# Performance work log

Hardware: AMD Instinct MI355X
Metric: run time of the kernel (lower is better)

Reference implementation:

```python
import jax, jax.numpy as jnp
import numpy as np

D = 46      # embed_dim, pinned by hardcoded repeat(1, 46, 1)
H = 256     # hidden_dim
H2 = 128    # hidden_dim // 2
L0 = 4000   # antigen length
L1 = 600    # antibody length
CAT = 250   # heavy/light chain split (catsite)
K_ECA = 3   # ECA conv1d kernel size for C=46
EPS = 1e-5


def _eca(x, w):
    # Standard ECA: global mean over spatial dims, conv1d across channel axis, sigmoid gate.
    spatial = tuple(range(2, x.ndim))
    y = x.mean(axis=spatial)  # [B, C]
    yc = jax.lax.conv_general_dilated(y[:, None, :], w[None, None, :], (1,), 'SAME')[:, 0, :]
    s = jax.nn.sigmoid(yc)
    return x * s.reshape(s.shape + (1,) * len(spatial))


def _bn(x, g, b):
    # BatchNorm2d, training mode (batch statistics, biased variance), affine.
    mu = x.mean(axis=(0, 2, 3), keepdims=True)
    var = ((x - mu) ** 2).mean(axis=(0, 2, 3), keepdims=True)
    return (x - mu) * jax.lax.rsqrt(var + EPS) * g[None, :, None, None] + b[None, :, None, None]


def _conv1x1(x, w, b):
    return jnp.einsum('bcij,oc->boij', x, w) + b[None, :, None, None]


def setup_inputs() -> dict:
    key = jax.random.key(0)
    ks = jax.random.split(key, 10)
    rng = np.random.default_rng(0)
    cdrH = np.sort(rng.choice(np.arange(1, CAT), 50, replace=False))            # CDR positions in heavy chain
    cdrLfull = np.sort(rng.choice(np.arange(CAT + 1, L1 - 1), 50, replace=False))
    inp = {
        'z0': jax.random.normal(ks[0], (1, L0, D), jnp.float32),
        'z1': jax.random.normal(ks[1], (1, L1, D), jnp.float32),
        'w_eca1': jax.random.normal(ks[2], (K_ECA,), jnp.float32) * 0.5,
        'w_eca2': jax.random.normal(ks[3], (K_ECA,), jnp.float32) * 0.5,
        'w_eca3': jax.random.normal(ks[4], (K_ECA,), jnp.float32) * 0.5,
        'w_eca4': jax.random.normal(ks[5], (K_ECA,), jnp.float32) * 0.5,
        'w_eca5': jax.random.normal(ks[6], (K_ECA,), jnp.float32) * 0.5,
        'conv_w': jax.random.normal(ks[7], (H, 2 * D), jnp.float32) / np.sqrt(2 * D).astype(np.float32),
        'conv_b': jnp.zeros((H,), jnp.float32),
        'bn_g': jnp.ones((H,), jnp.float32),
        'bn_b': jnp.zeros((H,), jnp.float32),
        'conv2_w': jax.random.normal(ks[8], (H2, H), jnp.float32) / np.sqrt(H).astype(np.float32),
        'conv2_b': jnp.zeros((H2,), jnp.float32),
        'bn2_g': jnp.ones((H2,), jnp.float32),
        'bn2_b': jnp.zeros((H2,), jnp.float32),
        'cdrHind': jnp.asarray(cdrH, jnp.int32),
        'cdrLind': jnp.asarray(cdrLfull - CAT, jnp.int32),
        'notcdrHind': jnp.asarray(np.setdiff1d(np.arange(CAT), cdrH), jnp.int32),
        'notcdrLind': jnp.asarray(np.setdiff1d(np.arange(CAT, L1 - 1), cdrLfull) - CAT, jnp.int32),
        'catsite': CAT,
    }
    return inp


def reference(z0, z1, w_eca1, w_eca2, w_eca3, w_eca4, w_eca5,
              conv_w, conv_b, bn_g, bn_b, conv2_w, conv2_b, bn2_g, bn2_b,
              cdrHind, cdrLind, notcdrHind, notcdrLind, catsite):
    z0 = z0.transpose(0, 2, 1)   # [1, D, L0]
    z1 = z1.transpose(0, 2, 1)   # [1, D, L1]
    z1H = z1[:, :, :catsite]     # [1, D, LH]
    z1L = z1[:, :, catsite:]     # [1, D, LL]

    z0 = _eca(z0, w_eca1)
    z1H = _eca(z1H, w_eca2)
    z1L = _eca(z1L, w_eca3)

    # Gather CDR / non-CDR residues along the length axis.
    Z1Hcdr = z1H[:, :, cdrHind]        # [1, D, nCH]
    Z1Hnot = z1H[:, :, notcdrHind]     # [1, D, nNH]
    Z1Lcdr = z1L[:, :, cdrLind]
    Z1Lnot = z1L[:, :, notcdrLind]

    # CDR vs non-CDR pairwise |diff|, ECA gate, mean over non-CDR axis.
    z_Hdifcdr = jnp.abs(Z1Hcdr[:, :, :, None] - Z1Hnot[:, :, None, :])  # [1, D, nCH, nNH]
    z1H = _eca(z_Hdifcdr, w_eca4).mean(axis=3)                          # [1, D, nCH]
    z_Ldifcdr = jnp.abs(Z1Lcdr[:, :, :, None] - Z1Lnot[:, :, None, :])
    z1L = _eca(z_Ldifcdr, w_eca5).mean(axis=3)                          # [1, D, nCL]

    # Antigen x heavy-CDR broadcast features.
    z_Hdif = jnp.abs(z0[:, :, :, None] - z1H[:, :, None, :])            # [1, D, L0, nCH]
    z_Hmul = z0[:, :, :, None] * z1H[:, :, None, :]
    z_Hcat = jnp.concatenate([z_Hdif, z_Hmul], axis=1)                  # [1, 2D, L0, nCH]
    z0_mean = z_Hcat.mean(axis=3)                                       # [1, 2D, L0]

    half = z0_mean.shape[1] // 2
    z0_Ldif = z0_mean[:, :half, :]
    z0_Lmul = z0_mean[:, half:, :]
    z_Ldif = jnp.abs(z0_Ldif[:, :, :, None] - z1L[:, :, None, :])       # [1, D, L0, nCL]
    z_Lmul = jnp.abs(z0_Lmul[:, :, :, None] - z1L[:, :, None, :])       # (abs of diff, as in source)
    z_Lcat = jnp.concatenate([z_Ldif, z_Lmul], axis=1)                  # [1, 2D, L0, nCL]

    z_cat = jnp.concatenate([z_Hcat, z_Lcat], axis=3)                   # [1, 2D, L0, nCH+nCL]

    c = jax.nn.relu(_conv1x1(z_cat, conv_w, conv_b))
    c = _bn(c, bn_g, bn_b)
    c = jax.nn.relu(_conv1x1(c, conv2_w, conv2_b))
    c = _bn(c, bn2_g, bn2_b)
    return c
```

## Files before the change

kernel.cpp:

```cpp
#include <hip/hip_runtime.h>
#include <math.h>

#define DD   46
#define LL0  4000
#define LL1  600
#define CATV 250
#define NC   50
#define NJ   100
#define HC   256
#define H2C  128
#define NPOS (LL0*NJ)
#define EPSV 1e-5f
#define NT   64
#define XROW 104
#define C1ROW 268
#define C2PAD 68
#define TILES (NPOS/NT)
#define GRIDP 512

#define W_MEAN0   0
#define W_MEANH   64
#define W_MEANL   128
#define W_RM4     192
#define W_RM5     256
#define W_S1      320
#define W_HBAR    384
#define W_RAWMH   448
#define W_RAWML   2752
#define W_H       5056
#define W_L       7360
#define W_BN1S    9664
#define W_SC1     10176
#define W_BN2S    10688
#define W_SC2     10944
#define W_HBF     11200
#define W_LBF     12400
#define W_AWT     13632
#define W_W1P     589776
#define W_W2BF    602064
#define W_BIAS2   618448

typedef __attribute__((ext_vector_type(8))) short bf8;
typedef __attribute__((ext_vector_type(4))) float f32x4;
typedef __attribute__((ext_vector_type(4))) unsigned u32x4;

__device__ __forceinline__ float sigf(float x){ return 1.0f/(1.0f+__expf(-x)); }

__device__ __forceinline__ unsigned short f2bf(float f){
  unsigned u = __float_as_uint(f);
  return (unsigned short)((u + 0x7FFFu + ((u>>16)&1u)) >> 16);
}
__device__ __forceinline__ unsigned pk2bf(float a, float b){
  return ((unsigned)f2bf(b)<<16) | (unsigned)f2bf(a);
}
__device__ __forceinline__ float bf2f(unsigned short h){
  return __uint_as_float(((unsigned)h)<<16);
}

__device__ float blockReduceSum(float v, float* sm){
  int tid=threadIdx.x;
  sm[tid]=v; __syncthreads();
  for(int s=128;s>0;s>>=1){ if(tid<s) sm[tid]+=sm[tid+s]; __syncthreads(); }
  float r=sm[0]; __syncthreads();
  return r;
}

__global__ void k_prep(const float* __restrict__ conv_w, float* __restrict__ ws){
  int t=blockIdx.x*256+threadIdx.x;
  if(blockIdx.x==0){ for(int e=threadIdx.x;e<1536;e+=256) ws[W_BN1S+e]=0.f; }
  if(t<HC*96){
    int o=t/96, c=t-o*96;
    unsigned short v=0;
    if(c<92){ int d=c>>1, p=c&1; v=f2bf(conv_w[o*92 + (p? 46+d : d)]); }
    ((unsigned short*)(ws+W_W1P))[t]=v;
  }
}

__global__ void k_prep2(const float* __restrict__ conv2_w, const float* __restrict__ conv2_b,
                        float* __restrict__ ws){
  __shared__ float sm[256];
  int o2=blockIdx.x, t=threadIdx.x;
  float wv=conv2_w[o2*HC+t];
  float sc=ws[W_SC1+t], sh=ws[W_SC1+HC+t];
  ((unsigned short*)(ws+W_W2BF))[o2*HC+t]=f2bf(wv*sc);
  float r=blockReduceSum(wv*sh,sm);
  if(t==0) ws[W_BIAS2+o2]=conv2_b[o2]+r;
}

__global__ void k_means(const float* __restrict__ z0, const float* __restrict__ z1,
                        const int* cdrH, const int* notH,
                        const int* cdrL, const int* notL,
                        int nCdrH,int nNotH,int nCdrL,int nNotL, float* ws){
  __shared__ float v[LL1];
  __shared__ float sm[256];
  int d=blockIdx.x, tid=threadIdx.x;
  float s0=0.f; for(int i=tid;i<LL0;i+=256) s0+=z0[i*DD+d];
  for(int k=tid;k<LL1;k+=256) v[k]=z1[k*DD+d];
  float r0=blockReduceSum(s0,sm);
  __syncthreads();
  float sH=0.f; for(int k=tid;k<CATV;k+=256) sH+=v[k];
  float sL=0.f; for(int k=CATV+tid;k<LL1;k+=256) sL+=v[k];
  float rH=blockReduceSum(sH,sm);
  float rL=blockReduceSum(sL,sm);
  float partH=0.f, partL=0.f;
  for(int i=tid;i<nCdrH;i+=256){
    float c=v[cdrH[i]]; float s=0.f;
    for(int j=0;j<nNotH;j++) s+=fabsf(c-v[notH[j]]);
    s/= (float)nNotH;
    ws[W_RAWMH+d*NC+i]=s; partH+=s;
  }
  for(int i=tid;i<nCdrL;i+=256){
    float c=v[CATV+cdrL[i]]; float s=0.f;
    for(int j=0;j<nNotL;j++) s+=fabsf(c-v[CATV+notL[j]]);
    s/= (float)nNotL;
    ws[W_RAWML+d*NC+i]=s; partL+=s;
  }
  float pH=blockReduceSum(partH,sm);
  float pL=blockReduceSum(partL,sm);
  if(tid==0){
    ws[W_MEAN0+d]=r0/(float)LL0;
    ws[W_MEANH+d]=rH/(float)CATV;
    ws[W_MEANL+d]=rL/(float)(LL1-CATV);
    ws[W_RM4+d]=pH/(float)nCdrH;
    ws[W_RM5+d]=pL/(float)nCdrL;
  }
}

__device__ __forceinline__ float conv3(const float* a, int d, const float* w){
  float acc = w[1]*a[d];
  if(d>0)    acc += w[0]*a[d-1];
  if(d<DD-1) acc += w[2]*a[d+1];
  return acc;
}

__global__ void k_scales(const float* w1,const float* w2,const float* w3,
                         const float* w4,const float* w5, float* ws){
  __shared__ float m0[DD], mH[DD], mL[DD];
  __shared__ float s1s[DD],s2s[DD],s3s[DD],s4s[DD],s5s[DD],y4[DD],y5[DD];
  int tid=threadIdx.x;
  if(tid<DD){ m0[tid]=ws[W_MEAN0+tid]; mH[tid]=ws[W_MEANH+tid]; mL[tid]=ws[W_MEANL+tid]; }
  __syncthreads();
  if(tid<DD){
    s1s[tid]=sigf(conv3(m0,tid,w1));
    s2s[tid]=sigf(conv3(mH,tid,w2));
    s3s[tid]=sigf(conv3(mL,tid,w3));
  }
  __syncthreads();
  if(tid<DD){ y4[tid]=s2s[tid]*ws[W_RM4+tid]; y5[tid]=s3s[tid]*ws[W_RM5+tid]; }
  __syncthreads();
  if(tid<DD){
    s4s[tid]=sigf(conv3(y4,tid,w4));
    s5s[tid]=sigf(conv3(y5,tid,w5));
    ws[W_S1+tid]=s1s[tid];
  }
  __syncthreads();
  for(int e=tid;e<DD*NC;e+=256){
    int d=e/NC;
    ws[W_H+e]=s4s[d]*s2s[d]*ws[W_RAWMH+e];
    ws[W_L+e]=s5s[d]*s3s[d]*ws[W_RAWML+e];
  }
  __syncthreads();
  if(tid<DD){
    float s=0.f;
    for(int j=0;j<NC;j++) s+=ws[W_H+tid*NC+j];
    ws[W_HBAR+tid]=s/(float)NC;
  }
  __syncthreads();
  for(int e=tid;e<2400;e+=256){
    int j=e/48, d=e-48*j;
    unsigned short hv=0, lv=0;
    if(d<DD){ hv=f2bf(ws[W_H+d*NC+j]); lv=f2bf(ws[W_L+d*NC+j]); }
    ((unsigned short*)(ws+W_HBF))[e]=hv;
    ((unsigned short*)(ws+W_LBF))[e]=lv;
  }
}

__global__ void k_aw(const float* __restrict__ z0, float* __restrict__ ws){
  int e=blockIdx.x*256+threadIdx.x;
  if(e>=LL0*48) return;
  int i=e/48, d=e-48*i;
  float a=0.f, df=0.f, ml=0.f;
  if(d<DD){
    a = ws[W_S1+d]*z0[i*DD+d];
    float s=0.f;
    #pragma unroll 10
    for(int j=0;j<NC;j++) s+=fabsf(a-ws[W_H+d*NC+j]);
    df = s*(1.0f/(float)NC);
    ml = a*ws[W_HBAR+d];
  }
  ws[W_AWT + i*144 + d]      = a;
  ws[W_AWT + i*144 + 48 + d] = df;
  ws[W_AWT + i*144 + 96 + d] = ml;
}

__device__ __forceinline__ void stage_tables(unsigned short* hT, unsigned short* lT,
                                             const float* __restrict__ ws, int tid){
  for(int e=tid;e<300;e+=256){
    ((u32x4*)hT)[e]=((const u32x4*)(ws+W_HBF))[e];
    ((u32x4*)lT)[e]=((const u32x4*)(ws+W_LBF))[e];
  }
}

__device__ __forceinline__ void build_X(unsigned short* Xl, const float* aw,
                                        const unsigned short* hT, const unsigned short* lT,
                                        int n0, int i0, int tid){
  int ibase=i0*100, ib1=ibase+100;
  for(int e=tid;e<NT*12;e+=256){
    int n=e/12, g=e-12*n, d4=g*4;
    int ncol=n0+n;
    int ii=(ncol>=ib1)?1:0;
    int j=ncol-ibase-ii*100;
    const float* ar=aw+ii*144;
    float x10,x11,x12,x13, x20,x21,x22,x23;
    if(j<NC){
      float4 a=*(const float4*)(ar+d4);
      ushort4 hb=*(const ushort4*)(hT+j*48+d4);
      float h0=bf2f(hb.x),h1=bf2f(hb.y),h2=bf2f(hb.z),h3=bf2f(hb.w);
      x10=fabsf(a.x-h0); x20=a.x*h0;
      x11=fabsf(a.y-h1); x21=a.y*h1;
      x12=fabsf(a.z-h2); x22=a.z*h2;
      x13=fabsf(a.w-h3); x23=a.w*h3;
    }else{
      float4 df=*(const float4*)(ar+48+d4);
      float4 ml=*(const float4*)(ar+96+d4);
      ushort4 lb=*(const ushort4*)(lT+(j-NC)*48+d4);
      float l0=bf2f(lb.x),l1=bf2f(lb.y),l2=bf2f(lb.z),l3=bf2f(lb.w);
      x10=fabsf(df.x-l0); x20=fabsf(ml.x-l0);
      x11=fabsf(df.y-l1); x21=fabsf(ml.y-l1);
      x12=fabsf(df.z-l2); x22=fabsf(ml.z-l2);
      x13=fabsf(df.w-l3); x23=fabsf(ml.w-l3);
    }
    u32x4 pv;
    pv.x=pk2bf(x10,x20); pv.y=pk2bf(x11,x21); pv.z=pk2bf(x12,x22); pv.w=pk2bf(x13,x23);
    *(u32x4*)(Xl + n*XROW + 8*g) = pv;
  }
}

__global__ __launch_bounds__(256,2) void k_gemmA(const float* __restrict__ ws,
                                                 const float* __restrict__ conv_b,
                                                 float* __restrict__ bnsum){
  __shared__ unsigned short hT[2400], lT[2400];
  __shared__ float aw[2][288];
  __shared__ unsigned short Xl[NT*XROW];
  __shared__ float bnred[512];
  int tid=threadIdx.x;
  int l=tid&63, w=tid>>6, lr=l&15, hi=l>>4, mb=w*64;
  stage_tables(hT,lT,ws,tid);
  const unsigned short* W1p=(const unsigned short*)(ws+W_W1P);
  bf8 w1f[4][3];
  #pragma unroll
  for(int tm=0;tm<4;tm++)
    #pragma unroll
    for(int ks=0;ks<3;ks++)
      w1f[tm][ks]=*(const bf8*)(W1p + (mb+tm*16+lr)*96 + ks*32 + hi*8);
  float bb[4][4];
  #pragma unroll
  for(int tm=0;tm<4;tm++)
    #pragma unroll
    for(int r=0;r<4;r++) bb[tm][r]=conv_b[mb+tm*16+hi*4+r];
  float s[4][4], q[4][4];
  #pragma unroll
  for(int tm=0;tm<4;tm++)
    #pragma unroll
    for(int r=0;r<4;r++){ s[tm][r]=0.f; q[tm][r]=0.f; }
  if(tid<72) ((float4*)aw[0])[tid]=*(((const float4*)(ws+W_AWT+((blockIdx.x*NT)/100)*144))+tid);
  __syncthreads();

  int pb=0;
  for(int t=blockIdx.x;t<TILES;t+=GRIDP){
    int n0=t*NT, i0=n0/100, nxt=t+GRIDP;
    build_X(Xl,aw[pb],hT,lT,n0,i0,tid);
    __syncthreads();
    if(tid<72 && nxt<TILES)
      ((float4*)aw[pb^1])[tid]=*(((const float4*)(ws+W_AWT+((nxt*NT)/100)*144))+tid);
    f32x4 acc[4][4];
    #pragma unroll
    for(int tm=0;tm<4;tm++)
      #pragma unroll
      for(int tn=0;tn<4;tn++) acc[tm][tn]=(f32x4){0.f,0.f,0.f,0.f};
    #pragma unroll
    for(int ks=0;ks<3;ks++){
      bf8 b[4];
      #pragma unroll
      for(int tn=0;tn<4;tn++)
        b[tn]=*(const bf8*)(Xl + (tn*16+lr)*XROW + ks*32 + hi*8);
      #pragma unroll
      for(int tm=0;tm<4;tm++)
        #pragma unroll
        for(int tn=0;tn<4;tn++)
          acc[tm][tn]=__builtin_amdgcn_mfma_f32_16x16x32_bf16(w1f[tm][ks],b[tn],acc[tm][tn],0,0,0);
    }
    #pragma unroll
    for(int tm=0;tm<4;tm++)
      #pragma unroll
      for(int tn=0;tn<4;tn++)
        #pragma unroll
        for(int r=0;r<4;r++){
          float vv=fmaxf(acc[tm][tn][r]+bb[tm][r],0.f);
          s[tm][r]+=vv; q[tm][r]+=vv*vv;
        }
    __syncthreads();
    pb^=1;
  }
  #pragma unroll
  for(int m=1;m<16;m<<=1)
    #pragma unroll
    for(int tm=0;tm<4;tm++)
      #pragma unroll
      for(int r=0;r<4;r++){
        s[tm][r]+=__shfl_xor(s[tm][r],m);
        q[tm][r]+=__shfl_xor(q[tm][r],m);
      }
  if(lr==0){
    #pragma unroll
    for(int tm=0;tm<4;tm++)
      #pragma unroll
      for(int r=0;r<4;r++){
        int o=mb+tm*16+hi*4+r;
        bnred[o]=s[tm][r]; bnred[256+o]=q[tm][r];
      }
  }
  __syncthreads();
  for(int e=tid;e<512;e+=256) atomicAdd(&bnsum[e],bnred[e]);
}

__global__ void k_bnparams(float* ws, const float* g, const float* b,
                           int nch, int sumoff, int scoff){
  int o=threadIdx.x;
  if(o<nch){
    float mu =ws[sumoff+o]    *(1.0f/(float)NPOS);
    float ex2=ws[sumoff+nch+o]*(1.0f/(float)NPOS);
    float var=ex2-mu*mu; if(var<0.f) var=0.f;
    float sc=g[o]*rsqrtf(var+EPSV);
    ws[scoff+o]=sc;
    ws[scoff+nch+o]=b[o]-mu*sc;
  }
}

__global__ __launch_bounds__(256,2) void k_gemmB(const float* __restrict__ ws,
      const float* __restrict__ conv_b, float* __restrict__ out,
      float* __restrict__ bn2sum){
  __shared__ unsigned short hT[2400], lT[2400];
  __shared__ float aw[2][288];
  __shared__ unsigned short BUF[NT*C1ROW];
  __shared__ float bnred[256];
  int tid=threadIdx.x;
  int l=tid&63, w=tid>>6, lr=l&15, hi=l>>4, mb=w*64, mb2=w*32;
  stage_tables(hT,lT,ws,tid);
  const unsigned short* W1p =(const unsigned short*)(ws+W_W1P);
  const unsigned short* W2bf=(const unsigned short*)(ws+W_W2BF);
  const float* bias2=ws+W_BIAS2;
  unsigned* outu=(unsigned*)out;
  bf8 w1f[4][3];
  #pragma unroll
  for(int tm=0;tm<4;tm++)
    #pragma unroll
    for(int ks=0;ks<3;ks++)
      w1f[tm][ks]=*(const bf8*)(W1p + (mb+tm*16+lr)*96 + ks*32 + hi*8);
  bf8 w2f[2][8];
  #pragma unroll
  for(int tm2=0;tm2<2;tm2++)
    #pragma unroll
    for(int ks=0;ks<8;ks++)
      w2f[tm2][ks]=*(const bf8*)(W2bf + (mb2+tm2*16+lr)*HC + ks*32 + hi*8);
  float bb[4][4];
  #pragma unroll
  for(int tm=0;tm<4;tm++)
    #pragma unroll
    for(int r=0;r<4;r++) bb[tm][r]=conv_b[mb+tm*16+hi*4+r];
  float bb2[2][4];
  #pragma unroll
  for(int tm2=0;tm2<2;tm2++)
    #pragma unroll
    for(int r=0;r<4;r++) bb2[tm2][r]=bias2[mb2+tm2*16+hi*4+r];
  float s2[2][4], q2[2][4];
  #pragma unroll
  for(int tm2=0;tm2<2;tm2++)
    #pragma unroll
    for(int r=0;r<4;r++){ s2[tm2][r]=0.f; q2[tm2][r]=0.f; }
  if(tid<72) ((float4*)aw[0])[tid]=*(((const float4*)(ws+W_AWT+((blockIdx.x*NT)/100)*144))+tid);
  __syncthreads();

  int pb=0;
  for(int t=blockIdx.x;t<TILES;t+=GRIDP){
    int n0=t*NT, i0=n0/100, nxt=t+GRIDP;
    build_X(BUF,aw[pb],hT,lT,n0,i0,tid);
    __syncthreads();
    if(tid<72 && nxt<TILES)
      ((float4*)aw[pb^1])[tid]=*(((const float4*)(ws+W_AWT+((nxt*NT)/100)*144))+tid);
    f32x4 acc[4][4];
    #pragma unroll
    for(int tm=0;tm<4;tm++)
      #pragma unroll
      for(int tn=0;tn<4;tn++) acc[tm][tn]=(f32x4){0.f,0.f,0.f,0.f};
    #pragma unroll
    for(int ks=0;ks<3;ks++){
      bf8 b[4];
      #pragma unroll
      for(int tn=0;tn<4;tn++)
        b[tn]=*(const bf8*)(BUF + (tn*16+lr)*XROW + ks*32 + hi*8);
      #pragma unroll
      for(int tm=0;tm<4;tm++)
        #pragma unroll
        for(int tn=0;tn<4;tn++)
          acc[tm][tn]=__builtin_amdgcn_mfma_f32_16x16x32_bf16(w1f[tm][ks],b[tn],acc[tm][tn],0,0,0);
    }
    __syncthreads();
    #pragma unroll
    for(int tm=0;tm<4;tm++)
      #pragma unroll
      for(int tn=0;tn<4;tn++){
        int n=tn*16+lr, ob=mb+tm*16+hi*4;
        float v0=fmaxf(acc[tm][tn][0]+bb[tm][0],0.f);
        float v1=fmaxf(acc[tm][tn][1]+bb[tm][1],0.f);
        float v2=fmaxf(acc[tm][tn][2]+bb[tm][2],0.f);
        float v3=fmaxf(acc[tm][tn][3]+bb[tm][3],0.f);
        uint2 pv; pv.x=pk2bf(v0,v1); pv.y=pk2bf(v2,v3);
        *(uint2*)&BUF[n*C1ROW+ob]=pv;
      }
    __syncthreads();
    f32x4 acc2[2][4];
    #pragma unroll
    for(int tm2=0;tm2<2;tm2++)
      #pragma unroll
      for(int tn=0;tn<4;tn++) acc2[tm2][tn]=(f32x4){0.f,0.f,0.f,0.f};
    #pragma unroll
    for(int ks=0;ks<8;ks++){
      bf8 b2[4];
      #pragma unroll
      for(int tn=0;tn<4;tn++)
        b2[tn]=*(const bf8*)(BUF + (tn*16+lr)*C1ROW + ks*32 + hi*8);
      #pragma unroll
      for(int tm2=0;tm2<2;tm2++)
        #pragma unroll
        for(int tn=0;tn<4;tn++)
          acc2[tm2][tn]=__builtin_amdgcn_mfma_f32_16x16x32_bf16(w2f[tm2][ks],b2[tn],acc2[tm2][tn],0,0,0);
    }
    __syncthreads();
    unsigned* C2s=(unsigned*)BUF;
    #pragma unroll
    for(int tm2=0;tm2<2;tm2++)
      #pragma unroll
      for(int tn=0;tn<4;tn++){
        float v0=fmaxf(acc2[tm2][tn][0]+bb2[tm2][0],0.f);
        float v1=fmaxf(acc2[tm2][tn][1]+bb2[tm2][1],0.f);
        float v2=fmaxf(acc2[tm2][tn][2]+bb2[tm2][2],0.f);
        float v3=fmaxf(acc2[tm2][tn][3]+bb2[tm2][3],0.f);
        s2[tm2][0]+=v0; q2[tm2][0]+=v0*v0;
        s2[tm2][1]+=v1; q2[tm2][1]+=v1*v1;
        s2[tm2][2]+=v2; q2[tm2][2]+=v2*v2;
        s2[tm2][3]+=v3; q2[tm2][3]+=v3*v3;
        int n=tn*16+lr;
        int q0=(mb2+tm2*16+hi*4)>>1;
        C2s[q0*C2PAD+n]    =pk2bf(v0,v1);
        C2s[(q0+1)*C2PAD+n]=pk2bf(v2,v3);
      }
    __syncthreads();
    #pragma unroll
    for(int p16=0;p16<4;p16++){
      int row=p16*16+(tid>>4), chunk=tid&15;
      u32x4 v=*(const u32x4*)&C2s[row*C2PAD+chunk*4];
      *(u32x4*)(outu + (size_t)(2*row)*NPOS + n0 + chunk*4) = v;
    }
    __syncthreads();
    pb^=1;
  }
  #pragma unroll
  for(int m=1;m<16;m<<=1)
    #pragma unroll
    for(int tm2=0;tm2<2;tm2++)
      #pragma unroll
      for(int r=0;r<4;r++){
        s2[tm2][r]+=__shfl_xor(s2[tm2][r],m);
        q2[tm2][r]+=__shfl_xor(q2[tm2][r],m);
      }
  if(lr==0){
    #pragma unroll
    for(int tm2=0;tm2<2;tm2++)
      #pragma unroll
      for(int r=0;r<4;r++){
        int o=mb2+tm2*16+hi*4+r;
        bnred[o]=s2[tm2][r]; bnred[128+o]=q2[tm2][r];
      }
  }
  __syncthreads();
  if(tid<256) atomicAdd(&bn2sum[tid],bnred[tid]);
}

__global__ void k_passC(float* __restrict__ out, const float* __restrict__ ws){
  const int NQ4=NPOS/4;
  int idx=blockIdx.x*256+threadIdx.x;
  int stride=gridDim.x*256;
  unsigned* outu=(unsigned*)out;
  for(int e=idx;e<64*NQ4;e+=stride){
    int qq=e/NQ4, nb=(e-qq*NQ4)*4;
    size_t base=(size_t)(2*qq)*NPOS + nb;
    u32x4 v=__builtin_nontemporal_load((const u32x4*)(outu+base));
    float sc0=ws[W_SC2+2*qq],   sh0=ws[W_SC2+H2C+2*qq];
    float sc1=ws[W_SC2+2*qq+1], sh1=ws[W_SC2+H2C+2*qq+1];
    f32x4 o0,o1;
    o0.x=bf2f((unsigned short)(v.x&0xffff))*sc0+sh0;
    o1.x=bf2f((unsigned short)(v.x>>16))  *sc1+sh1;
    o0.y=bf2f((unsigned short)(v.y&0xffff))*sc0+sh0;
    o1.y=bf2f((unsigned short)(v.y>>16))  *sc1+sh1;
    o0.z=bf2f((unsigned short)(v.z&0xffff))*sc0+sh0;
    o1.z=bf2f((unsigned short)(v.z>>16))  *sc1+sh1;
    o0.w=bf2f((unsigned short)(v.w&0xffff))*sc0+sh0;
    o1.w=bf2f((unsigned short)(v.w>>16))  *sc1+sh1;
    __builtin_nontemporal_store(o0,(f32x4*)(out+base));
    __builtin_nontemporal_store(o1,(f32x4*)(out+base+NPOS));
  }
}

extern "C" void kernel_launch(void* const* d_in, const int* in_sizes, int n_in,
                              void* d_out, int out_size, void* d_ws, size_t ws_size,
                              hipStream_t stream){
  const float* z0     =(const float*)d_in[0];
  const float* z1     =(const float*)d_in[1];
  const float* we1    =(const float*)d_in[2];
  const float* we2    =(const float*)d_in[3];
  const float* we3    =(const float*)d_in[4];
  const float* we4    =(const float*)d_in[5];
  const float* we5    =(const float*)d_in[6];
  const float* conv_w =(const float*)d_in[7];
  const float* conv_b =(const float*)d_in[8];
  const float* bn_g   =(const float*)d_in[9];
  const float* bn_b   =(const float*)d_in[10];
  const float* conv2_w=(const float*)d_in[11];
  const float* conv2_b=(const float*)d_in[12];
  const float* bn2_g  =(const float*)d_in[13];
  const float* bn2_b  =(const float*)d_in[14];
  const int* cdrH=(const int*)d_in[15];
  const int* cdrL=(const int*)d_in[16];
  const int* notH=(const int*)d_in[17];
  const int* notL=(const int*)d_in[18];
  int nCdrH=in_sizes[15], nCdrL=in_sizes[16], nNotH=in_sizes[17], nNotL=in_sizes[18];
  float* ws=(float*)d_ws;
  float* out=(float*)d_out;

  hipLaunchKernelGGL(k_prep,     dim3(96),   dim3(256),0,stream, conv_w,ws);
  hipLaunchKernelGGL(k_means,    dim3(DD),   dim3(256),0,stream, z0,z1,cdrH,notH,cdrL,notL,
                     nCdrH,nNotH,nCdrL,nNotL,ws);
  hipLaunchKernelGGL(k_scales,   dim3(1),    dim3(256),0,stream, we1,we2,we3,we4,we5,ws);
  hipLaunchKernelGGL(k_aw,       dim3((LL0*48+255)/256), dim3(256),0,stream, z0,ws);
  hipLaunchKernelGGL(k_gemmA,    dim3(GRIDP),dim3(256),0,stream, ws,conv_b, ws+W_BN1S);
  hipLaunchKernelGGL(k_bnparams, dim3(1),    dim3(256),0,stream, ws,bn_g,bn_b, HC, W_BN1S, W_SC1);
  hipLaunchKernelGGL(k_prep2,    dim3(H2C),  dim3(256),0,stream, conv2_w,conv2_b,ws);
  hipLaunchKernelGGL(k_gemmB,    dim3(GRIDP),dim3(256),0,stream, ws,conv_b, out, ws+W_BN2S);
  hipLaunchKernelGGL(k_bnparams, dim3(1),    dim3(256),0,stream, ws,bn2_g,bn2_b, H2C, W_BN2S, W_SC2);
  hipLaunchKernelGGL(k_passC,    dim3(2048), dim3(256),0,stream, out, ws);
}
```

Baseline: 233.4 us.

## Double-buffer the X tile and build the next tile during the current GEMM

The shared staging buffer is split into a double-buffered X tile and a separate C1/C2 buffer. Each iteration now builds the next tile's X operand while the first GEMM runs on the current one, and prefetches attention weights two tiles ahead. This removes one barrier per iteration and lets the scalar X construction interleave with MFMA work. In exchange, shared memory per block rises to roughly 74 KB, which with two blocks per CU approaches the LDS limit and adds register pressure from the interleaved code.

```diff
diff --git a/kernel.cpp b/kernel.cpp
--- a/kernel.cpp
+++ b/kernel.cpp
@@ -342,7 +342,8 @@
       float* __restrict__ bn2sum){
   __shared__ unsigned short hT[2400], lT[2400];
   __shared__ float aw[2][288];
-  __shared__ unsigned short BUF[NT*C1ROW];
+  __shared__ unsigned short Xl[2][NT*XROW];
+  __shared__ unsigned short C1s[NT*C1ROW];
   __shared__ float bnred[256];
   int tid=threadIdx.x;
   int l=tid&63, w=tid>>6, lr=l&15, hi=l>>4, mb=w*64, mb2=w*32;
@@ -378,16 +379,22 @@
   for(int tm2=0;tm2<2;tm2++)
     #pragma unroll
     for(int r=0;r<4;r++){ s2[tm2][r]=0.f; q2[tm2][r]=0.f; }
-  if(tid<72) ((float4*)aw[0])[tid]=*(((const float4*)(ws+W_AWT+((blockIdx.x*NT)/100)*144))+tid);
-  __syncthreads();
-
-  int pb=0;
+  {
+    int t0=blockIdx.x;
+    if(tid<72) ((float4*)aw[0])[tid]=*(((const float4*)(ws+W_AWT+((t0*NT)/100)*144))+tid);
+    __syncthreads();
+    build_X(Xl[0],aw[0],hT,lT,t0*NT,(t0*NT)/100,tid);
+    if(tid<72 && t0+GRIDP<TILES)
+      ((float4*)aw[1])[tid]=*(((const float4*)(ws+W_AWT+(((t0+GRIDP)*NT)/100)*144))+tid);
+    __syncthreads();
+  }
+
+  int p=0, qb=1;
   for(int t=blockIdx.x;t<TILES;t+=GRIDP){
-    int n0=t*NT, i0=n0/100, nxt=t+GRIDP;
-    build_X(BUF,aw[pb],hT,lT,n0,i0,tid);
-    __syncthreads();
-    if(tid<72 && nxt<TILES)
-      ((float4*)aw[pb^1])[tid]=*(((const float4*)(ws+W_AWT+((nxt*NT)/100)*144))+tid);
+    int n0=t*NT, nxt=t+GRIDP, nn2=t+2*GRIDP;
+    if(tid<72 && nn2<TILES)
+      ((float4*)aw[qb^1])[tid]=*(((const float4*)(ws+W_AWT+((nn2*NT)/100)*144))+tid);
+    if(nxt<TILES) build_X(Xl[p^1],aw[qb],hT,lT,nxt*NT,(nxt*NT)/100,tid);
     f32x4 acc[4][4];
     #pragma unroll
     for(int tm=0;tm<4;tm++)
@@ -398,7 +405,7 @@
       bf8 b[4];
       #pragma unroll
       for(int tn=0;tn<4;tn++)
-        b[tn]=*(const bf8*)(BUF + (tn*16+lr)*XROW + ks*32 + hi*8);
+        b[tn]=*(const bf8*)(Xl[p] + (tn*16+lr)*XROW + ks*32 + hi*8);
       #pragma unroll
       for(int tm=0;tm<4;tm++)
         #pragma unroll
@@ -416,7 +423,7 @@
         float v2=fmaxf(acc[tm][tn][2]+bb[tm][2],0.f);
         float v3=fmaxf(acc[tm][tn][3]+bb[tm][3],0.f);
         uint2 pv; pv.x=pk2bf(v0,v1); pv.y=pk2bf(v2,v3);
-        *(uint2*)&BUF[n*C1ROW+ob]=pv;
+        *(uint2*)&C1s[n*C1ROW+ob]=pv;
       }
     __syncthreads();
     f32x4 acc2[2][4];
@@ -429,7 +436,7 @@
       bf8 b2[4];
       #pragma unroll
       for(int tn=0;tn<4;tn++)
-        b2[tn]=*(const bf8*)(BUF + (tn*16+lr)*C1ROW + ks*32 + hi*8);
+        b2[tn]=*(const bf8*)(C1s + (tn*16+lr)*C1ROW + ks*32 + hi*8);
       #pragma unroll
       for(int tm2=0;tm2<2;tm2++)
         #pragma unroll
@@ -437,7 +444,7 @@
           acc2[tm2][tn]=__builtin_amdgcn_mfma_f32_16x16x32_bf16(w2f[tm2][ks],b2[tn],acc2[tm2][tn],0,0,0);
     }
     __syncthreads();
-    unsigned* C2s=(unsigned*)BUF;
+    unsigned* C2s=(unsigned*)C1s;
     #pragma unroll
     for(int tm2=0;tm2<2;tm2++)
       #pragma unroll
@@ -462,8 +469,7 @@
       u32x4 v=*(const u32x4*)&C2s[row*C2PAD+chunk*4];
       *(u32x4*)(outu + (size_t)(2*row)*NPOS + n0 + chunk*4) = v;
     }
-    __syncthreads();
-    pb^=1;
+    p^=1; qb^=1;
   }
   #pragma unroll
   for(int m=1;m<16;m<<=1)
```

Result: no change. 230.7 us (-1.2%).
